# Performance work log

Hardware: AMD Instinct MI355X
Metric: run time of the kernel (lower is better)

The kernel has to match this reference:

```python
import jax, jax.numpy as jnp
import numpy as np

N_NODES = 100000
N_TYPES = 7
N_EDGES = 400000
D = 128


def setup_inputs() -> dict:
    key = jax.random.key(0)
    k1, k2, k3, k4 = jax.random.split(key, 4)
    x = jax.random.normal(k1, (N_NODES, D), dtype=jnp.float32)
    edge_indices = jax.random.randint(k2, (N_TYPES, 2, N_EDGES), 0, N_NODES, dtype=jnp.int64)
    # per-type linear weights of the cloned base GNNs (scaled for stability)
    W = jax.random.normal(k3, (N_TYPES, D, D), dtype=jnp.float32) * (1.0 / np.sqrt(D))
    b = jax.random.normal(k4, (N_TYPES, D), dtype=jnp.float32) * 0.02
    return {"x": x, "edge_indices": edge_indices, "W": W, "b": b}


def _type_conv(x, src, dst, Wt, bt, n_nodes):
    # gather -> segment-mean aggregate -> linear, one edge type
    msg = x[src]                                                   # [E, D]
    summed = jax.ops.segment_sum(msg, dst, num_segments=n_nodes)   # [N, D]
    cnt = jax.ops.segment_sum(jnp.ones(src.shape, x.dtype), dst, num_segments=n_nodes)
    mean = summed / jnp.maximum(cnt, 1.0)[:, None]
    return mean @ Wt + bt


def reference(x, edge_indices, W, b):
    n_nodes = x.shape[0]
    n_types = edge_indices.shape[0]
    # loop over the small fixed set of edge types (structurally distinct GNNs)
    acc = jnp.zeros_like(x)
    for t in range(n_types):
        acc = acc + _type_conv(x, edge_indices[t, 0], edge_indices[t, 1], W[t], b[t], n_nodes)
    return acc / n_types
```

## Files before the change

### kernel.cpp

```cpp
#include <hip/hip_runtime.h>

#define N_NODES 100000
#define N_TYPES 7
#define N_EDGES 400000
#define DIM 128
#define NTOT (N_TYPES * N_NODES)
#define ETOT (N_TYPES * N_EDGES)

#define RBITS 10
#define RNODE 1024
#define NBUCK 98
#define BSTRIDE 128
#define CAP 6144
#define CHUNK 2048
#define NCHUNKS ((N_EDGES + CHUNK - 1) / CHUNK)

typedef short v8s __attribute__((ext_vector_type(8)));
typedef float v4f __attribute__((ext_vector_type(4)));

__device__ __forceinline__ unsigned short f2bf(float f) {
    unsigned int x = __float_as_uint(f);
    return (unsigned short)((x + 0x7FFFu + ((x >> 16) & 1u)) >> 16);
}

__global__ __launch_bounds__(256) void cast_x_kernel(
    const float* __restrict__ x, unsigned short* __restrict__ xb)
{
    int i = blockIdx.x * 256 + threadIdx.x;
    if (i >= N_NODES * DIM / 4) return;
    float4 v = reinterpret_cast<const float4*>(x)[i];
    ushort4 o;
    o.x = f2bf(v.x); o.y = f2bf(v.y); o.z = f2bf(v.z); o.w = f2bf(v.w);
    reinterpret_cast<ushort4*>(xb)[i] = o;
}

__global__ __launch_bounds__(256) void cast_wt_kernel(
    const float* __restrict__ W, unsigned short* __restrict__ WT)
{
    int i = blockIdx.x * 256 + threadIdx.x;
    if (i >= N_TYPES * DIM * DIM) return;
    int t = i >> 14, r = i & 16383, j = r >> 7, k = r & 127;
    WT[i] = f2bf(W[(t << 14) + (k << 7) + j]);
}

__global__ __launch_bounds__(128) void bsum_kernel(
    const float* __restrict__ b, float* __restrict__ bsum)
{
    int j = threadIdx.x;
    float s = 0.f;
    for (int t = 0; t < N_TYPES; ++t) s += b[t * DIM + j];
    bsum[j] = s;
}

__global__ __launch_bounds__(256) void binpass_kernel(
    const int* __restrict__ ei, int* __restrict__ gcur,
    unsigned int* __restrict__ bucketbuf)
{
    __shared__ unsigned int packedLds[CHUNK];
    __shared__ unsigned char bLds[CHUNK];
    __shared__ unsigned int sortedLds[CHUNK];
    __shared__ int cnt[BSTRIDE];
    __shared__ int lofs[BSTRIDE];
    __shared__ int gbase[BSTRIDE];

    const int blk = blockIdx.x;
    const int t = blk / NCHUNKS;
    const int c = blk - t * NCHUNKS;
    const int* srcp = ei + (size_t)t * 2 * N_EDGES;
    const int* dstp = srcp + N_EDGES;
    const int e0 = c * CHUNK;
    const int e1 = min(e0 + CHUNK, N_EDGES);
    const int tid = threadIdx.x;

    if (tid < BSTRIDE) cnt[tid] = 0;
    __syncthreads();

#pragma unroll
    for (int k = 0; k < CHUNK / 256; ++k) {
        int j = tid + k * 256;
        int e = e0 + j;
        unsigned char b = 0xFF;
        unsigned int pk = 0;
        if (e < e1) {
            int s = srcp[e];
            int d = dstp[e];
            b = (unsigned char)(d >> RBITS);
            pk = ((unsigned int)(d & (RNODE - 1)) << 17) | (unsigned int)s;
            atomicAdd(&cnt[b], 1);
        }
        packedLds[j] = pk;
        bLds[j] = b;
    }
    __syncthreads();

    if (tid < BSTRIDE) lofs[tid] = cnt[tid];
    __syncthreads();
    for (int off = 1; off < BSTRIDE; off <<= 1) {
        int tv = 0;
        if (tid >= off && tid < BSTRIDE) tv = lofs[tid - off];
        __syncthreads();
        if (tid < BSTRIDE) lofs[tid] += tv;
        __syncthreads();
    }
    if (tid < BSTRIDE) lofs[tid] -= cnt[tid];
    __syncthreads();

    if (tid < BSTRIDE) {
        int n = cnt[tid];
        int base = -1;
        if (n > 0 && tid < NBUCK) {
            int rel = atomicAdd(&gcur[t * BSTRIDE + tid], n);
            base = (t * BSTRIDE + tid) * CAP + rel;
        }
        gbase[tid] = base;
        cnt[tid] = lofs[tid];
    }
    __syncthreads();

#pragma unroll
    for (int k = 0; k < CHUNK / 256; ++k) {
        int j = tid + k * 256;
        unsigned char b = bLds[j];
        if (b != 0xFF) {
            int p = atomicAdd(&cnt[b], 1);
            sortedLds[p] = packedLds[j];
        }
    }
    __syncthreads();

    const int wave = tid >> 6, lane = tid & 63;
    for (int b = wave * 32; b < wave * 32 + 32; ++b) {
        if (b >= NBUCK) break;
        int base = gbase[b];
        if (base < 0) continue;
        int o = lofs[b];
        int n = cnt[b] - o;
        for (int i = lane; i < n; i += 64)
            bucketbuf[(size_t)base + i] = sortedLds[o + i];
    }
}

__global__ __launch_bounds__(256) void bucket_hist_kernel(
    const unsigned int* __restrict__ bucketbuf, const int* __restrict__ gcur,
    int* __restrict__ deg)
{
    __shared__ int cnt[RNODE];
    const int blk = blockIdx.x;
    const int t = blk / NBUCK;
    const int b = blk - t * NBUCK;
    const int n = min(gcur[t * BSTRIDE + b], CAP);
    const int g0 = b << RBITS;
    const int validR = min(RNODE, N_NODES - g0);
    const int tid = threadIdx.x;
    for (int j = tid; j < RNODE; j += 256) cnt[j] = 0;
    __syncthreads();
    const unsigned int* bb = bucketbuf + (size_t)(t * BSTRIDE + b) * CAP;
    for (int i = tid; i < n; i += 256)
        atomicAdd(&cnt[bb[i] >> 17], 1);
    __syncthreads();
    int* dg = deg + (size_t)t * N_NODES + g0;
    for (int j = tid; j < validR; j += 256) dg[j] = cnt[j];
}

__global__ __launch_bounds__(256) void scan1_kernel(
    const int* __restrict__ deg, int* __restrict__ offs, int* __restrict__ bsum)
{
    __shared__ int s[256];
    int tid = threadIdx.x;
    int base = blockIdx.x * 1024 + tid * 4;
    int v[4];
    int tot = 0;
#pragma unroll
    for (int j = 0; j < 4; ++j) {
        v[j] = (base + j < NTOT) ? deg[base + j] : 0;
        tot += v[j];
    }
    s[tid] = tot;
    __syncthreads();
    for (int off = 1; off < 256; off <<= 1) {
        int t2 = (tid >= off) ? s[tid - off] : 0;
        __syncthreads();
        s[tid] += t2;
        __syncthreads();
    }
    if (tid == 255) bsum[blockIdx.x] = s[255];
    int run = s[tid] - tot;
#pragma unroll
    for (int j = 0; j < 4; ++j) {
        if (base + j < NTOT) offs[base + j] = run;
        run += v[j];
    }
}

__global__ __launch_bounds__(1024) void scan2_kernel(int* __restrict__ bsum, int nb)
{
    __shared__ int s[1024];
    int tid = threadIdx.x;
    int v = (tid < nb) ? bsum[tid] : 0;
    s[tid] = v;
    __syncthreads();
    for (int off = 1; off < 1024; off <<= 1) {
        int t2 = (tid >= off) ? s[tid - off] : 0;
        __syncthreads();
        s[tid] += t2;
        __syncthreads();
    }
    if (tid < nb) bsum[tid] = s[tid] - v;
}

__global__ __launch_bounds__(256) void scan3_kernel(
    int* __restrict__ offs, const int* __restrict__ bsum)
{
    int i = blockIdx.x * 256 + threadIdx.x;
    if (i < NTOT) offs[i] += bsum[i >> 10];
    if (i == 0) offs[NTOT] = ETOT;
}

__global__ __launch_bounds__(256) void place_kernel(
    const unsigned int* __restrict__ bucketbuf, const int* __restrict__ gcur,
    const int* __restrict__ offs, int* __restrict__ srcperm)
{
    __shared__ int cur[RNODE];
    __shared__ int sorted[CAP];
    const int blk = blockIdx.x;
    const int t = blk / NBUCK;
    const int b = blk - t * NBUCK;
    const int n = min(gcur[t * BSTRIDE + b], CAP);
    const int g0 = b << RBITS;
    const int validR = min(RNODE, N_NODES - g0);
    const int tid = threadIdx.x;
    const int* offt = offs + (size_t)t * N_NODES + g0;
    const int base0 = offt[0];
    for (int j = tid; j < validR; j += 256) cur[j] = offt[j] - base0;
    __syncthreads();
    const unsigned int* bb = bucketbuf + (size_t)(t * BSTRIDE + b) * CAP;
    for (int i = tid; i < n; i += 256) {
        unsigned int pk = bb[i];
        int p = atomicAdd(&cur[pk >> 17], 1);
        sorted[p] = (int)(pk & 0x1FFFFu);
    }
    __syncthreads();
    int* outp = srcperm + base0;
    for (int i = tid; i < n; i += 256) outp[i] = sorted[i];
}

__global__ __launch_bounds__(256) void aggregate_kernel(
    const unsigned short* __restrict__ xb,
    const int* __restrict__ offs,
    const int* __restrict__ srcperm,
    unsigned short* __restrict__ meanout,
    int grp0, int ngrp)
{
    int gi = blockIdx.x * 16 + (threadIdx.x >> 4);
    if (gi >= ngrp) return;
    int grp = grp0 + gi;
    int l = threadIdx.x & 15;

    int beg = offs[grp];
    int end = offs[grp + 1];
    int m = end - beg;

    int mm = m;
    mm = max(mm, __shfl_xor(mm, 16));
    mm = max(mm, __shfl_xor(mm, 32));

    float a[8];
#pragma unroll
    for (int j = 0; j < 8; ++j) a[j] = 0.f;

    const int eSafe = min(beg, ETOT - 1);
#pragma unroll 2
    for (int i = 0; i < mm; ++i) {
        bool valid = i < m;
        int e = valid ? (beg + i) : eSafe;
        int s = srcperm[e];
        uint4 v = *reinterpret_cast<const uint4*>(
            reinterpret_cast<const char*>(xb) + ((size_t)s << 8) + (l << 4));
        float w = valid ? 1.f : 0.f;
        a[0] += w * __uint_as_float(v.x << 16);
        a[1] += w * __uint_as_float(v.x & 0xFFFF0000u);
        a[2] += w * __uint_as_float(v.y << 16);
        a[3] += w * __uint_as_float(v.y & 0xFFFF0000u);
        a[4] += w * __uint_as_float(v.z << 16);
        a[5] += w * __uint_as_float(v.z & 0xFFFF0000u);
        a[6] += w * __uint_as_float(v.w << 16);
        a[7] += w * __uint_as_float(v.w & 0xFFFF0000u);
    }

    float inv = 1.0f / fmaxf((float)m, 1.0f);
    unsigned int p0, p1, p2, p3;
    asm("v_cvt_pk_bf16_f32 %0, %1, %2" : "=v"(p0) : "v"(a[0] * inv), "v"(a[1] * inv));
    asm("v_cvt_pk_bf16_f32 %0, %1, %2" : "=v"(p1) : "v"(a[2] * inv), "v"(a[3] * inv));
    asm("v_cvt_pk_bf16_f32 %0, %1, %2" : "=v"(p2) : "v"(a[4] * inv), "v"(a[5] * inv));
    asm("v_cvt_pk_bf16_f32 %0, %1, %2" : "=v"(p3) : "v"(a[6] * inv), "v"(a[7] * inv));
    uint4 o = make_uint4(p0, p1, p2, p3);
    *reinterpret_cast<uint4*>(
        reinterpret_cast<char*>(meanout) + ((size_t)gi << 8) + (l << 4)) = o;
}

__global__ __launch_bounds__(256) void matmul_kernel(
    const unsigned short* __restrict__ meanall, size_t meanStride,
    int t0, int nt,
    const unsigned short* __restrict__ WT,
    const float* __restrict__ bsum,
    float* __restrict__ out, int accum)
{
    __shared__ unsigned short sB[DIM * DIM];

    const int tid = threadIdx.x;
    const int wave = tid >> 6;
    const int lane = tid & 63;
    const int rlo = lane & 15;
    const int khi = lane >> 4;
    const int row0 = blockIdx.x * 64 + wave * 16;

    v4f acc[8];
#pragma unroll
    for (int n = 0; n < 8; ++n) acc[n] = (v4f){0.f, 0.f, 0.f, 0.f};

    for (int tt = 0; tt < nt; ++tt) {
        int t = t0 + tt;
        __syncthreads();
        const uint4* gw = reinterpret_cast<const uint4*>(WT + ((size_t)t << 14));
#pragma unroll
        for (int i = 0; i < 8; ++i) {
            int c = tid + (i << 8);
            uint4 v = gw[c];
            int L = c << 4;
            int row = L >> 8;
            int sb = (row << 8) | ((L & 255) ^ ((row & 7) << 4));
            *reinterpret_cast<uint4*>(reinterpret_cast<char*>(sB) + sb) = v;
        }
        __syncthreads();

        int rowA = row0 + rlo;
        if (rowA >= N_NODES) rowA = N_NODES - 1;
        const unsigned short* arow = meanall + (size_t)tt * meanStride + ((size_t)rowA << 7);

#pragma unroll
        for (int k0 = 0; k0 < DIM; k0 += 32) {
            v8s a = *reinterpret_cast<const v8s*>(arow + k0 + (khi << 3));
#pragma unroll
            for (int n = 0; n < 8; ++n) {
                int jrow = (n << 4) | rlo;
                int kb = (k0 + (khi << 3)) << 1;
                int sb = (jrow << 8) | (kb ^ ((jrow & 7) << 4));
                v8s bf = *reinterpret_cast<const v8s*>(reinterpret_cast<char*>(sB) + sb);
                acc[n] = __builtin_amdgcn_mfma_f32_16x16x32_bf16(a, bf, acc[n], 0, 0, 0);
            }
        }
    }

    const float inv7 = 1.0f / 7.0f;
#pragma unroll
    for (int n = 0; n < 8; ++n) {
        int col = (n << 4) | rlo;
        float bs = bsum[col];
#pragma unroll
        for (int r = 0; r < 4; ++r) {
            int row = row0 + (khi << 2) + r;
            if (row < N_NODES) {
                float* p = out + ((size_t)row << 7) + col;
                if (accum) *p += acc[n][r] * inv7;
                else       *p = (acc[n][r] + bs) * inv7;
            }
        }
    }
}

__global__ __launch_bounds__(256) void out_init_kernel(
    const float* __restrict__ bsum, float* __restrict__ out)
{
    int i = blockIdx.x * 256 + threadIdx.x;
    if (i >= N_NODES * DIM / 4) return;
    int c4 = (i & 31) * 4;
    const float inv7 = 1.0f / 7.0f;
    float4 bv = *reinterpret_cast<const float4*>(bsum + c4);
    float4 o = make_float4(bv.x * inv7, bv.y * inv7, bv.z * inv7, bv.w * inv7);
    reinterpret_cast<float4*>(out)[i] = o;
}

extern "C" void kernel_launch(void* const* d_in, const int* in_sizes, int n_in,
                              void* d_out, int out_size, void* d_ws, size_t ws_size,
                              hipStream_t stream) {
    const float* x  = (const float*)d_in[0];
    const int*   ei = (const int*)d_in[1];
    const float* W  = (const float*)d_in[2];
    const float* b  = (const float*)d_in[3];
    float* out = (float*)d_out;

    char* p = (char*)d_ws;
    unsigned short* xb = (unsigned short*)p;          p += (size_t)N_NODES * DIM * 2;
    unsigned short* WT = (unsigned short*)p;          p += (size_t)N_TYPES * DIM * DIM * 2;
    float* bsum = (float*)p;                          p += 512;
    int* srcperm = (int*)p;                           p += (size_t)ETOT * 4;
    int* deg = (int*)p;                               p += (size_t)NTOT * 4;
    int* offs = (int*)p;                              p += (size_t)(NTOT + 1) * 4;
    int* bscan = (int*)p;                             p += 1024 * 4;
    int* gcur = (int*)p;                              p += (size_t)N_TYPES * BSTRIDE * 4;
    p = (char*)(((uintptr_t)p + 15) & ~(uintptr_t)15);
    unsigned short* meanbuf = (unsigned short*)p;
    unsigned int* bucketbuf = (unsigned int*)p;
    size_t mean1_bytes = (size_t)N_NODES * DIM * 2;
    size_t used = (size_t)(p - (char*)d_ws);
    bool fused = (ws_size >= used + 7 * mean1_bytes);

    const int NB = (NTOT + 1023) / 1024;

    cast_x_kernel<<<(N_NODES * DIM / 4 + 255) / 256, 256, 0, stream>>>(x, xb);
    cast_wt_kernel<<<(N_TYPES * DIM * DIM + 255) / 256, 256, 0, stream>>>(W, WT);
    bsum_kernel<<<1, 128, 0, stream>>>(b, bsum);

    hipMemsetAsync(gcur, 0, (size_t)N_TYPES * BSTRIDE * 4, stream);
    binpass_kernel<<<N_TYPES * NCHUNKS, 256, 0, stream>>>(ei, gcur, bucketbuf);
    bucket_hist_kernel<<<N_TYPES * NBUCK, 256, 0, stream>>>(bucketbuf, gcur, deg);
    scan1_kernel<<<NB, 256, 0, stream>>>(deg, offs, bscan);
    scan2_kernel<<<1, 1024, 0, stream>>>(bscan, NB);
    scan3_kernel<<<(NTOT + 255) / 256, 256, 0, stream>>>(offs, bscan);
    place_kernel<<<N_TYPES * NBUCK, 256, 0, stream>>>(bucketbuf, gcur, offs, srcperm);

    const int matmul_blocks = (N_NODES + 63) / 64;

    if (fused) {
        size_t meanStride = (size_t)N_NODES * DIM;
        aggregate_kernel<<<(NTOT + 15) / 16, 256, 0, stream>>>(
            xb, offs, srcperm, meanbuf, 0, NTOT);
        matmul_kernel<<<matmul_blocks, 256, 0, stream>>>(
            meanbuf, meanStride, 0, N_TYPES, WT, bsum, out, 0);
    } else {
        out_init_kernel<<<(N_NODES * DIM / 4 + 255) / 256, 256, 0, stream>>>(bsum, out);
        for (int t = 0; t < N_TYPES; ++t) {
            aggregate_kernel<<<(N_NODES + 15) / 16, 256, 0, stream>>>(
                xb, offs, srcperm, meanbuf, t * N_NODES, N_NODES);
            matmul_kernel<<<matmul_blocks, 256, 0, stream>>>(
                meanbuf, 0, t, 1, WT, bsum, out, 1);
        }
    }
}
```

Before: 250.0 us.

## Degree-sort aggregation groups, fuse histogram with scan, read weights directly from global

Adds a per-chunk counting sort of destination groups by in-degree, so the 16-lane groups that share a wavefront have similar loop trip counts, which reduces divergence in the aggregate loop. Fuses the bucket histogram with the first-level prefix scan per bucket, which removes the deg buffer and one launch. Merges the bias-sum into the weight-cast kernel. The matmul now reads transposed weights straight from global or cache instead of staging them in LDS, which trades LDS traffic and barriers for uncached-friendly global loads. The sort adds an extra pass and breaks locality of the destination rows that aggregate writes.

After: 467.1 us. 86.9% more time.

```diff
diff --git a/kernel.cpp b/kernel.cpp
--- a/kernel.cpp
+++ b/kernel.cpp
@@ -15,6 +15,9 @@
 #define CHUNK 2048
 #define NCHUNKS ((N_EDGES + CHUNK - 1) / CHUNK)
 
+#define DG 4096
+#define NCLS 64
+
 typedef short v8s __attribute__((ext_vector_type(8)));
 typedef float v4f __attribute__((ext_vector_type(4)));
 
@@ -34,22 +37,23 @@
     reinterpret_cast<ushort4*>(xb)[i] = o;
 }
 
-__global__ __launch_bounds__(256) void cast_wt_kernel(
-    const float* __restrict__ W, unsigned short* __restrict__ WT)
-{
+__global__ __launch_bounds__(256) void cast_wt_bsum_kernel(
+    const float* __restrict__ W, const float* __restrict__ b,
+    unsigned short* __restrict__ WT, float* __restrict__ bsum)
+{
+    if (blockIdx.x == 448) {
+        int j = threadIdx.x;
+        if (j < DIM) {
+            float s = 0.f;
+            for (int t = 0; t < N_TYPES; ++t) s += b[t * DIM + j];
+            bsum[j] = s;
+        }
+        return;
+    }
     int i = blockIdx.x * 256 + threadIdx.x;
     if (i >= N_TYPES * DIM * DIM) return;
     int t = i >> 14, r = i & 16383, j = r >> 7, k = r & 127;
     WT[i] = f2bf(W[(t << 14) + (k << 7) + j]);
-}
-
-__global__ __launch_bounds__(128) void bsum_kernel(
-    const float* __restrict__ b, float* __restrict__ bsum)
-{
-    int j = threadIdx.x;
-    float s = 0.f;
-    for (int t = 0; t < N_TYPES; ++t) s += b[t * DIM + j];
-    bsum[j] = s;
 }
 
 __global__ __launch_bounds__(256) void binpass_kernel(
@@ -140,11 +144,12 @@
     }
 }
 
-__global__ __launch_bounds__(256) void bucket_hist_kernel(
+__global__ __launch_bounds__(256) void bucket_hist_scan_kernel(
     const unsigned int* __restrict__ bucketbuf, const int* __restrict__ gcur,
-    int* __restrict__ deg)
+    int* __restrict__ offs, int* __restrict__ bscan)
 {
     __shared__ int cnt[RNODE];
+    __shared__ int s[256];
     const int blk = blockIdx.x;
     const int t = blk / NBUCK;
     const int b = blk - t * NBUCK;
@@ -158,23 +163,10 @@
     for (int i = tid; i < n; i += 256)
         atomicAdd(&cnt[bb[i] >> 17], 1);
     __syncthreads();
-    int* dg = deg + (size_t)t * N_NODES + g0;
-    for (int j = tid; j < validR; j += 256) dg[j] = cnt[j];
-}
-
-__global__ __launch_bounds__(256) void scan1_kernel(
-    const int* __restrict__ deg, int* __restrict__ offs, int* __restrict__ bsum)
-{
-    __shared__ int s[256];
-    int tid = threadIdx.x;
-    int base = blockIdx.x * 1024 + tid * 4;
-    int v[4];
-    int tot = 0;
-#pragma unroll
-    for (int j = 0; j < 4; ++j) {
-        v[j] = (base + j < NTOT) ? deg[base + j] : 0;
-        tot += v[j];
-    }
+    int base4 = tid * 4;
+    int v[4], tot = 0;
+#pragma unroll
+    for (int k = 0; k < 4; ++k) { v[k] = cnt[base4 + k]; tot += v[k]; }
     s[tid] = tot;
     __syncthreads();
     for (int off = 1; off < 256; off <<= 1) {
@@ -183,13 +175,14 @@
         s[tid] += t2;
         __syncthreads();
     }
-    if (tid == 255) bsum[blockIdx.x] = s[255];
     int run = s[tid] - tot;
-#pragma unroll
-    for (int j = 0; j < 4; ++j) {
-        if (base + j < NTOT) offs[base + j] = run;
-        run += v[j];
-    }
+    int* og = offs + (size_t)t * N_NODES + g0;
+#pragma unroll
+    for (int k = 0; k < 4; ++k) {
+        if (base4 + k < validR) og[base4 + k] = run;
+        run += v[k];
+    }
+    if (tid == 255) bscan[t * NBUCK + b] = s[255];
 }
 
 __global__ __launch_bounds__(1024) void scan2_kernel(int* __restrict__ bsum, int nb)
@@ -209,10 +202,14 @@
 }
 
 __global__ __launch_bounds__(256) void scan3_kernel(
-    int* __restrict__ offs, const int* __restrict__ bsum)
+    int* __restrict__ offs, const int* __restrict__ bscan)
 {
     int i = blockIdx.x * 256 + threadIdx.x;
-    if (i < NTOT) offs[i] += bsum[i >> 10];
+    if (i < NTOT) {
+        int t = i / N_NODES;
+        int r = i - t * N_NODES;
+        offs[i] += bscan[t * NBUCK + (r >> RBITS)];
+    }
     if (i == 0) offs[NTOT] = ETOT;
 }
 
@@ -244,16 +241,66 @@
     for (int i = tid; i < n; i += 256) outp[i] = sorted[i];
 }
 
+__global__ __launch_bounds__(256) void degsort_kernel(
+    const int* __restrict__ offs, int* __restrict__ perm)
+{
+    __shared__ int cnt[NCLS];
+    __shared__ int lofs[NCLS];
+    __shared__ unsigned char cls[DG];
+    __shared__ int sorted[DG];
+    const int tid = threadIdx.x;
+    const int g0 = blockIdx.x * DG;
+    const int nvalid = min(DG, NTOT - g0);
+
+    if (tid < NCLS) cnt[tid] = 0;
+    __syncthreads();
+    for (int j = tid; j < DG; j += 256) {
+        unsigned char c = 0xFF;
+        if (j < nvalid) {
+            int g = g0 + j;
+            int d = offs[g + 1] - offs[g];
+            c = (unsigned char)min(d, NCLS - 1);
+            atomicAdd(&cnt[c], 1);
+        }
+        cls[j] = c;
+    }
+    __syncthreads();
+    if (tid < NCLS) lofs[tid] = cnt[tid];
+    __syncthreads();
+    for (int off = 1; off < NCLS; off <<= 1) {
+        int tv = 0;
+        if (tid >= off && tid < NCLS) tv = lofs[tid - off];
+        __syncthreads();
+        if (tid < NCLS) lofs[tid] += tv;
+        __syncthreads();
+    }
+    if (tid < NCLS) {
+        lofs[tid] -= cnt[tid];
+        cnt[tid] = lofs[tid];
+    }
+    __syncthreads();
+    for (int j = tid; j < DG; j += 256) {
+        unsigned char c = cls[j];
+        if (c != 0xFF) {
+            int p = atomicAdd(&cnt[c], 1);
+            sorted[p] = g0 + j;
+        }
+    }
+    __syncthreads();
+    for (int j = tid; j < nvalid; j += 256) perm[g0 + j] = sorted[j];
+}
+
 __global__ __launch_bounds__(256) void aggregate_kernel(
     const unsigned short* __restrict__ xb,
     const int* __restrict__ offs,
     const int* __restrict__ srcperm,
+    const int* __restrict__ perm,
     unsigned short* __restrict__ meanout,
     int grp0, int ngrp)
 {
     int gi = blockIdx.x * 16 + (threadIdx.x >> 4);
     if (gi >= ngrp) return;
-    int grp = grp0 + gi;
+    int grp = perm ? perm[gi] : (grp0 + gi);
     int l = threadIdx.x & 15;
 
     int beg = offs[grp];
@@ -295,7 +342,7 @@
     asm("v_cvt_pk_bf16_f32 %0, %1, %2" : "=v"(p3) : "v"(a[6] * inv), "v"(a[7] * inv));
     uint4 o = make_uint4(p0, p1, p2, p3);
     *reinterpret_cast<uint4*>(
-        reinterpret_cast<char*>(meanout) + ((size_t)gi << 8) + (l << 4)) = o;
+        reinterpret_cast<char*>(meanout) + ((size_t)(grp - grp0) << 8) + (l << 4)) = o;
 }
 
 __global__ __launch_bounds__(256) void matmul_kernel(
@@ -305,8 +352,6 @@
     const float* __restrict__ bsum,
     float* __restrict__ out, int accum)
 {
-    __shared__ unsigned short sB[DIM * DIM];
-
     const int tid = threadIdx.x;
     const int wave = tid >> 6;
     const int lane = tid & 63;
@@ -318,34 +363,20 @@
 #pragma unroll
     for (int n = 0; n < 8; ++n) acc[n] = (v4f){0.f, 0.f, 0.f, 0.f};
 
+    int rowA = row0 + rlo;
+    if (rowA >= N_NODES) rowA = N_NODES - 1;
+
     for (int tt = 0; tt < nt; ++tt) {
         int t = t0 + tt;
-        __syncthreads();
-        const uint4* gw = reinterpret_cast<const uint4*>(WT + ((size_t)t << 14));
-#pragma unroll
-        for (int i = 0; i < 8; ++i) {
-            int c = tid + (i << 8);
-            uint4 v = gw[c];
-            int L = c << 4;
-            int row = L >> 8;
-            int sb = (row << 8) | ((L & 255) ^ ((row & 7) << 4));
-            *reinterpret_cast<uint4*>(reinterpret_cast<char*>(sB) + sb) = v;
-        }
-        __syncthreads();
-
-        int rowA = row0 + rlo;
-        if (rowA >= N_NODES) rowA = N_NODES - 1;
+        const unsigned short* wt = WT + ((size_t)t << 14);
         const unsigned short* arow = meanall + (size_t)tt * meanStride + ((size_t)rowA << 7);
-
 #pragma unroll
         for (int k0 = 0; k0 < DIM; k0 += 32) {
             v8s a = *reinterpret_cast<const v8s*>(arow + k0 + (khi << 3));
 #pragma unroll
             for (int n = 0; n < 8; ++n) {
-                int jrow = (n << 4) | rlo;
-                int kb = (k0 + (khi << 3)) << 1;
-                int sb = (jrow << 8) | (kb ^ ((jrow & 7) << 4));
-                v8s bf = *reinterpret_cast<const v8s*>(reinterpret_cast<char*>(sB) + sb);
+                int col = (n << 4) | rlo;
+                v8s bf = *reinterpret_cast<const v8s*>(wt + (col << 7) + k0 + (khi << 3));
                 acc[n] = __builtin_amdgcn_mfma_f32_16x16x32_bf16(a, bf, acc[n], 0, 0, 0);
             }
         }
@@ -394,44 +425,43 @@
     unsigned short* WT = (unsigned short*)p;          p += (size_t)N_TYPES * DIM * DIM * 2;
     float* bsum = (float*)p;                          p += 512;
     int* srcperm = (int*)p;                           p += (size_t)ETOT * 4;
-    int* deg = (int*)p;                               p += (size_t)NTOT * 4;
     int* offs = (int*)p;                              p += (size_t)(NTOT + 1) * 4;
+    int* perm = (int*)p;                              p += (size_t)NTOT * 4;
     int* bscan = (int*)p;                             p += 1024 * 4;
     int* gcur = (int*)p;                              p += (size_t)N_TYPES * BSTRIDE * 4;
     p = (char*)(((uintptr_t)p + 15) & ~(uintptr_t)15);
+    unsigned int* bucketbuf = (unsigned int*)p;
     unsigned short* meanbuf = (unsigned short*)p;
-    unsigned int* bucketbuf = (unsigned int*)p;
     size_t mean1_bytes = (size_t)N_NODES * DIM * 2;
     size_t used = (size_t)(p - (char*)d_ws);
-    bool fused = (ws_size >= used + 7 * mean1_bytes);
-
-    const int NB = (NTOT + 1023) / 1024;
+    size_t bucket_bytes = (size_t)N_TYPES * BSTRIDE * CAP * 4;
+    bool fused = (ws_size >= used + 7 * mean1_bytes) &&
+                 (7 * mean1_bytes >= bucket_bytes);
 
     cast_x_kernel<<<(N_NODES * DIM / 4 + 255) / 256, 256, 0, stream>>>(x, xb);
-    cast_wt_kernel<<<(N_TYPES * DIM * DIM + 255) / 256, 256, 0, stream>>>(W, WT);
-    bsum_kernel<<<1, 128, 0, stream>>>(b, bsum);
+    cast_wt_bsum_kernel<<<449, 256, 0, stream>>>(W, b, WT, bsum);
 
     hipMemsetAsync(gcur, 0, (size_t)N_TYPES * BSTRIDE * 4, stream);
     binpass_kernel<<<N_TYPES * NCHUNKS, 256, 0, stream>>>(ei, gcur, bucketbuf);
-    bucket_hist_kernel<<<N_TYPES * NBUCK, 256, 0, stream>>>(bucketbuf, gcur, deg);
-    scan1_kernel<<<NB, 256, 0, stream>>>(deg, offs, bscan);
-    scan2_kernel<<<1, 1024, 0, stream>>>(bscan, NB);
+    bucket_hist_scan_kernel<<<N_TYPES * NBUCK, 256, 0, stream>>>(bucketbuf, gcur, offs, bscan);
+    scan2_kernel<<<1, 1024, 0, stream>>>(bscan, N_TYPES * NBUCK);
     scan3_kernel<<<(NTOT + 255) / 256, 256, 0, stream>>>(offs, bscan);
     place_kernel<<<N_TYPES * NBUCK, 256, 0, stream>>>(bucketbuf, gcur, offs, srcperm);
+    degsort_kernel<<<(NTOT + DG - 1) / DG, 256, 0, stream>>>(offs, perm);
 
     const int matmul_blocks = (N_NODES + 63) / 64;
 
     if (fused) {
         size_t meanStride = (size_t)N_NODES * DIM;
         aggregate_kernel<<<(NTOT + 15) / 16, 256, 0, stream>>>(
-            xb, offs, srcperm, meanbuf, 0, NTOT);
+            xb, offs, srcperm, perm, meanbuf, 0, NTOT);
         matmul_kernel<<<matmul_blocks, 256, 0, stream>>>(
             meanbuf, meanStride, 0, N_TYPES, WT, bsum, out, 0);
     } else {
         out_init_kernel<<<(N_NODES * DIM / 4 + 255) / 256, 256, 0, stream>>>(bsum, out);
         for (int t = 0; t < N_TYPES; ++t) {
             aggregate_kernel<<<(N_NODES + 15) / 16, 256, 0, stream>>>(
-                xb, offs, srcperm, meanbuf, t * N_NODES, N_NODES);
+                xb, offs, srcperm, (const int*)nullptr, meanbuf, t * N_NODES, N_NODES);
             matmul_kernel<<<matmul_blocks, 256, 0, stream>>>(
                 meanbuf, 0, t, 1, WT, bsum, out, 1);
         }
```
